# Performance work log

Measured on AMD Instinct MI355X. Metric: run time of the kernel, lower is better.

## Reference

```python
import jax, jax.numpy as jnp
import numpy as np

DIM = 1024
NUM_PATTERNS = 8192
B, S = 2, 4096


def setup_inputs() -> dict:
    key = jax.random.key(0)
    k1, k2, k3 = jax.random.split(key, 3)
    scale = 1.0 / np.sqrt(DIM)
    x = jax.random.normal(k1, (B, S, DIM), dtype=jnp.float32)
    # nn.Linear default init ~ U(-1/sqrt(in), 1/sqrt(in)); normal*scale is fine for a baseline
    w_q = jax.random.normal(k2, (DIM, DIM), dtype=jnp.float32) * scale
    xi = jax.random.normal(k3, (NUM_PATTERNS, DIM), dtype=jnp.float32) * scale
    beta = jnp.float32(1.0 / np.sqrt(DIM))
    return {"x": x, "w_q": w_q, "xi": xi, "beta": beta}


def reference(x, w_q, xi, beta):
    # q = x @ w_q.T  (torch F.linear convention: weight is [out, in])
    q = jnp.einsum("bsd,ed->bse", x, w_q)
    # logits = beta * q @ xi.T  -> [B, S, P]
    logits = beta * jnp.einsum("bsd,pd->bsp", q, xi)
    attn = jax.nn.softmax(logits, axis=-1)
    # retrieve patterns: attn @ xi -> [B, S, dim]
    return jnp.einsum("bsp,pd->bsd", attn, xi)
```

## Files before the change

kernel.cpp:

```cpp
#include <hip/hip_runtime.h>


typedef __attribute__((ext_vector_type(4))) int int4v;
typedef __attribute__((ext_vector_type(8))) int int8v;
typedef __attribute__((ext_vector_type(4))) float f32x4;

#define NDIM 1024
#define NPAT 8192
#define NROW 8192

__device__ __forceinline__ unsigned f8pack4(float a, float b, float c, float d) {
  int w = __builtin_amdgcn_cvt_pk_fp8_f32(a, b, 0, false);
  w = __builtin_amdgcn_cvt_pk_fp8_f32(c, d, w, true);
  return (unsigned)w;
}
__device__ __forceinline__ unsigned char f8b(float v) {
  return (unsigned char)(__builtin_amdgcn_cvt_pk_fp8_f32(v, v, 0, false) & 0xff);
}
__device__ __forceinline__ int sig(int c) {
  return (c & 64) | ((c & 15) << 2) | ((c >> 4) & 3);
}
__device__ __forceinline__ long bpack_addr(int line, int s, int kt, int nkt) {
  return (((long)(line >> 4) * nkt + kt) * 2 + ((s >> 4) & 1)) * 1024 +
         ((s >> 5) * 16 + (line & 15)) * 16 + (s & 15);
}


__global__ void cast_pack(const float* __restrict__ in,
                          unsigned char* __restrict__ out, float scale) {
  int i = blockIdx.x * blockDim.x + threadIdx.x;
  int rw = i >> 8, d = (i & 255) * 4;
  float4 v = ((const float4*)in)[i];
  unsigned w = f8pack4(v.x * scale, v.y * scale, v.z * scale, v.w * scale);
  *(unsigned*)(out + bpack_addr(rw, d & 127, d >> 7, NDIM >> 7)) = w;
}

__global__ void xi_prep8(const float* __restrict__ xi,
                         unsigned char* __restrict__ xi8,
                         unsigned char* __restrict__ xit8,
                         float* __restrict__ colsum) {
  __shared__ float t[32][33];
  __shared__ float cs[8][32];
  int tx = threadIdx.x, ty = threadIdx.y;
  int d0 = blockIdx.x * 32, p0 = blockIdx.y * 32;
  int d = d0 + tx;
  const int s2 = sig(d & 127), kt2 = d >> 7;
  float psum = 0.f;
#pragma unroll
  for (int j = 0; j < 32; j += 8) {
    int p = p0 + ty + j;
    float v = xi[(long)p * NDIM + d];
    t[ty + j][tx] = v;
    psum += v;
    xi8[bpack_addr(p, s2, kt2, NDIM >> 7)] = f8b(32.f * v);
  }
  cs[ty][tx] = psum;
  __syncthreads();
  if (ty == 0) {
    float s = 0.f;
#pragma unroll
    for (int k = 0; k < 8; ++k) s += cs[k][tx];
    atomicAdd(&colsum[d0 + tx], s);
  }
  int p = p0 + tx;
  const int s3 = sig(p & 127), kt3 = p >> 7;
#pragma unroll
  for (int j = 0; j < 32; j += 8)
    xit8[bpack_addr(d0 + ty + j, s3, kt3, NPAT >> 7)] = f8b(32.f * t[tx][ty + j]);
}


#define MFMA1(D, AF, BF) \
  D = __builtin_amdgcn_mfma_scale_f32_16x16x128_f8f6f4( \
      AF, BF, D, 0, 0, 0, 0x7f7f7f7f, 0, 0x7f7f7f7f);

#define KBODY(KT, CURA, CURB, NXTA, NXTB)                                   \
  {                                                                         \
    const long o1 = ((KT) + 1 < nkt) ? 2048 : 0;                            \
    _Pragma("unroll") for (int t = 0; t < 4; ++t) {                         \
      int4v alo = *(const int4v*)(pAf[t] + o1);                             \
      int4v ahi = *(const int4v*)(pAf[t] + o1 + 1024);                      \
      NXTA[t] = __builtin_shufflevector(alo, ahi, 0, 1, 2, 3, 4, 5, 6, 7);  \
      int4v blo = *(const int4v*)(pBf[t] + o1);                             \
      int4v bhi = *(const int4v*)(pBf[t] + o1 + 1024);                      \
      NXTB[t] = __builtin_shufflevector(blo, bhi, 0, 1, 2, 3, 4, 5, 6, 7);  \
    }                                                                       \
    __builtin_amdgcn_s_setprio(1);                                          \
    _Pragma("unroll") for (int mt = 0; mt < 4; ++mt)                        \
      _Pragma("unroll") for (int nt = 0; nt < 4; ++nt)                      \
        MFMA1(acc[mt][nt], CURA[mt], CURB[nt])                              \
    __builtin_amdgcn_s_setprio(0);                                          \
    _Pragma("unroll") for (int t = 0; t < 4; ++t) {                         \
      pAf[t] += 2048;                                                       \
      pBf[t] += 2048;                                                       \
    }                                                                       \
  }

template <int MODE>
__launch_bounds__(256, 2)
__global__ void gemm_f8(const unsigned char* __restrict__ Ap,
                        const unsigned char* __restrict__ Bp,
                        void* __restrict__ Cv, int N, int K,
                        const float* __restrict__ beta_ptr,
                        const float* __restrict__ rowsum,
                        const float* __restrict__ colsum,
                        float* __restrict__ rowsum_out) {
  const int tid = threadIdx.x;
  const int wave = tid >> 6;
  const int lane = tid & 63;
  const int quad = lane >> 4, ln = lane & 15;

  const int nct = N >> 6;
  const int ct = blockIdx.x % nct;
  const int rt4 = blockIdx.x / nct;
  const long row0 = ((long)rt4 * 4 + wave) * 64;
  const long col0 = (long)ct * 64;
  const int nkt = K >> 7;

  const unsigned char* pAf[4];
  const unsigned char* pBf[4];
#pragma unroll
  for (int t = 0; t < 4; ++t) {
    pAf[t] = Ap + ((long)((int)(row0 >> 4) + t) * nkt) * 2048 + lane * 16;
    pBf[t] = Bp + ((long)((int)(col0 >> 4) + t) * nkt) * 2048 + lane * 16;
  }

  f32x4 acc[4][4] = {};
  int8v aC[4], bC[4], aN[4], bN[4];

#pragma unroll
  for (int t = 0; t < 4; ++t) {
    int4v alo = *(const int4v*)(pAf[t]);
    int4v ahi = *(const int4v*)(pAf[t] + 1024);
    aC[t] = __builtin_shufflevector(alo, ahi, 0, 1, 2, 3, 4, 5, 6, 7);
    int4v blo = *(const int4v*)(pBf[t]);
    int4v bhi = *(const int4v*)(pBf[t] + 1024);
    bC[t] = __builtin_shufflevector(blo, bhi, 0, 1, 2, 3, 4, 5, 6, 7);
  }

  for (int kt = 0; kt < nkt; kt += 2) {
    KBODY(kt, aC, bC, aN, bN)
    KBODY(kt + 1, aN, bN, aC, bC)
  }

  if (MODE == 0 || MODE == 1) {
    unsigned char* C8 = (unsigned char*)Cv;
    const int s0 = (int)(col0 & 64) + 4 * ln;
    const int kc = (int)(col0 >> 7);
    const int onk = N >> 7;
    if (MODE == 0) {
      const float s = 1.0f / 32.0f;
#pragma unroll
      for (int mt = 0; mt < 4; ++mt)
#pragma unroll
        for (int r = 0; r < 4; ++r) {
          int row = (int)row0 + mt * 16 + quad * 4 + r;
          unsigned w = f8pack4(acc[mt][0][r] * s, acc[mt][1][r] * s,
                               acc[mt][2][r] * s, acc[mt][3][r] * s);
          *(unsigned*)(C8 + bpack_addr(row, s0, kc, onk)) = w;
        }
    } else {
      const float bs = beta_ptr[0] * (1.0f / 32.0f);
#pragma unroll
      for (int mt = 0; mt < 4; ++mt)
#pragma unroll
        for (int r = 0; r < 4; ++r) {
          int row = (int)row0 + mt * 16 + quad * 4 + r;
          float e0 = (__expf(bs * acc[mt][0][r]) - 1.0f) * 32.f;
          float e1 = (__expf(bs * acc[mt][1][r]) - 1.0f) * 32.f;
          float e2 = (__expf(bs * acc[mt][2][r]) - 1.0f) * 32.f;
          float e3 = (__expf(bs * acc[mt][3][r]) - 1.0f) * 32.f;
          *(unsigned*)(C8 + bpack_addr(row, s0, kc, onk)) =
              f8pack4(e0, e1, e2, e3);
          float sm = e0 + e1 + e2 + e3;
          sm += __shfl_xor(sm, 1, 64);
          sm += __shfl_xor(sm, 2, 64);
          sm += __shfl_xor(sm, 4, 64);
          sm += __shfl_xor(sm, 8, 64);
          if (ln == 0) atomicAdd(&rowsum_out[row], sm);
        }
    }
  } else {
    float* C = (float*)Cv;
#pragma unroll
    for (int mt = 0; mt < 4; ++mt)
#pragma unroll
      for (int r = 0; r < 4; ++r) {
        long row = row0 + mt * 16 + quad * 4 + r;
        float inv = 1.0f / (8192.0f + rowsum[row] * (1.0f / 32.0f));
#pragma unroll
        for (int nt = 0; nt < 4; ++nt) {
          long col = col0 + nt * 16 + ln;
          C[row * N + col] =
              (acc[mt][nt][r] * (1.0f / 1024.0f) + colsum[col]) * inv;
        }
      }
  }
}


extern "C" void kernel_launch(void* const* d_in, const int* in_sizes, int n_in,
                              void* d_out, int out_size, void* d_ws,
                              size_t ws_size, hipStream_t stream) {
  const float* x    = (const float*)d_in[0];
  const float* wq   = (const float*)d_in[1];
  const float* xi   = (const float*)d_in[2];
  const float* beta = (const float*)d_in[3];
  float* out = (float*)d_out;

  char* ws = (char*)d_ws;
  const size_t MB = 1024 * 1024;
  unsigned char* x8   = (unsigned char*)(ws);
  unsigned char* wq8  = (unsigned char*)(ws + 8 * MB);
  unsigned char* q8   = (unsigned char*)(ws + 9 * MB);
  unsigned char* xi8  = (unsigned char*)(ws + 17 * MB);
  unsigned char* xit8 = (unsigned char*)(ws + 25 * MB);
  float*         rs   = (float*)(ws + 33 * MB);
  float*         csum = (float*)(ws + 33 * MB + 32768);
  unsigned char* E8   = (unsigned char*)(ws + 34 * MB);

  hipMemsetAsync(rs, 0, 36864, stream);

  cast_pack<<<(NROW * NDIM / 4) / 256, 256, 0, stream>>>(x, x8, 1.0f);
  cast_pack<<<(NDIM * NDIM / 4) / 256, 256, 0, stream>>>(wq, wq8, 32.0f);
  xi_prep8<<<dim3(NDIM / 32, NPAT / 32), dim3(32, 8), 0, stream>>>(
      xi, xi8, xit8, csum);

  gemm_f8<0><<<(NROW / 256) * (NDIM / 64), 256, 0, stream>>>(
      x8, wq8, q8, NDIM, NDIM, nullptr, nullptr, nullptr, nullptr);

  gemm_f8<1><<<(NROW / 256) * (NPAT / 64), 256, 0, stream>>>(
      q8, xi8, E8, NPAT, NDIM, beta, nullptr, nullptr, rs);

  gemm_f8<2><<<(NROW / 256) * (NDIM / 64), 256, 0, stream>>>(
      E8, xit8, out, NDIM, NPAT, nullptr, rs, csum, nullptr);
}
```

Before: 379.9 us.

## Repack fp8 tiles for 32-byte per-lane loads and XCD-aware block mapping

Changes the packed fp8 operand layout so each lane's 32 bytes for one MFMA k-tile are contiguous. Two 16-byte loads plus a shuffle become a single 32-byte vector load. Also remaps blockIdx so that blocks landing on the same XCD share row tiles and a group of column tiles, which should improve L2 reuse of A and B. The remap hardcodes a grid decomposition (8 XCDs, 32 row-groups, 8-column groups) that only fits particular N and M sizes.

```diff
diff --git a/kernel.cpp b/kernel.cpp
--- a/kernel.cpp
+++ b/kernel.cpp
@@ -1,7 +1,6 @@
 #include <hip/hip_runtime.h>
 
 
-typedef __attribute__((ext_vector_type(4))) int int4v;
 typedef __attribute__((ext_vector_type(8))) int int8v;
 typedef __attribute__((ext_vector_type(4))) float f32x4;
 
@@ -21,8 +20,8 @@
   return (c & 64) | ((c & 15) << 2) | ((c >> 4) & 3);
 }
 __device__ __forceinline__ long bpack_addr(int line, int s, int kt, int nkt) {
-  return (((long)(line >> 4) * nkt + kt) * 2 + ((s >> 4) & 1)) * 1024 +
-         ((s >> 5) * 16 + (line & 15)) * 16 + (s & 15);
+  return ((long)(line >> 4) * nkt + kt) * 2048 +
+         (((s >> 5) << 4) + (line & 15)) * 32 + (s & 31);
 }
 
 
@@ -78,12 +77,8 @@
   {                                                                         \
     const long o1 = ((KT) + 1 < nkt) ? 2048 : 0;                            \
     _Pragma("unroll") for (int t = 0; t < 4; ++t) {                         \
-      int4v alo = *(const int4v*)(pAf[t] + o1);                             \
-      int4v ahi = *(const int4v*)(pAf[t] + o1 + 1024);                      \
-      NXTA[t] = __builtin_shufflevector(alo, ahi, 0, 1, 2, 3, 4, 5, 6, 7);  \
-      int4v blo = *(const int4v*)(pBf[t] + o1);                             \
-      int4v bhi = *(const int4v*)(pBf[t] + o1 + 1024);                      \
-      NXTB[t] = __builtin_shufflevector(blo, bhi, 0, 1, 2, 3, 4, 5, 6, 7);  \
+      NXTA[t] = *(const int8v*)(pAf[t] + o1);                               \
+      NXTB[t] = *(const int8v*)(pBf[t] + o1);                               \
     }                                                                       \
     __builtin_amdgcn_s_setprio(1);                                          \
     _Pragma("unroll") for (int mt = 0; mt < 4; ++mt)                        \
@@ -110,9 +105,14 @@
   const int lane = tid & 63;
   const int quad = lane >> 4, ln = lane & 15;
 
-  const int nct = N >> 6;
-  const int ct = blockIdx.x % nct;
-  const int rt4 = blockIdx.x / nct;
+  const int xcd = blockIdx.x & 7;
+  const int idx = blockIdx.x >> 3;
+  const int ct_in = idx & 7;
+  const int rt4_loc = (idx >> 3) & 3;
+  const int c_outer = idx >> 5;
+  const int rt4 = xcd * 4 + rt4_loc;
+  const int ct = c_outer * 8 + ct_in;
+
   const long row0 = ((long)rt4 * 4 + wave) * 64;
   const long col0 = (long)ct * 64;
   const int nkt = K >> 7;
@@ -121,8 +121,8 @@
   const unsigned char* pBf[4];
 #pragma unroll
   for (int t = 0; t < 4; ++t) {
-    pAf[t] = Ap + ((long)((int)(row0 >> 4) + t) * nkt) * 2048 + lane * 16;
-    pBf[t] = Bp + ((long)((int)(col0 >> 4) + t) * nkt) * 2048 + lane * 16;
+    pAf[t] = Ap + ((long)((int)(row0 >> 4) + t) * nkt) * 2048 + lane * 32;
+    pBf[t] = Bp + ((long)((int)(col0 >> 4) + t) * nkt) * 2048 + lane * 32;
   }
 
   f32x4 acc[4][4] = {};
@@ -130,12 +130,8 @@
 
 #pragma unroll
   for (int t = 0; t < 4; ++t) {
-    int4v alo = *(const int4v*)(pAf[t]);
-    int4v ahi = *(const int4v*)(pAf[t] + 1024);
-    aC[t] = __builtin_shufflevector(alo, ahi, 0, 1, 2, 3, 4, 5, 6, 7);
-    int4v blo = *(const int4v*)(pBf[t]);
-    int4v bhi = *(const int4v*)(pBf[t] + 1024);
-    bC[t] = __builtin_shufflevector(blo, bhi, 0, 1, 2, 3, 4, 5, 6, 7);
+    aC[t] = *(const int8v*)(pAf[t]);
+    bC[t] = *(const int8v*)(pBf[t]);
   }
 
   for (int kt = 0; kt < nkt; kt += 2) {
```

New measurement: 324.5 us. -14.6%, faster.
